# Performance work log

Measured on AMD Instinct MI355X. Metric: run time of the kernel, lower is better.

Reference implementation:

```python
import jax, jax.numpy as jnp
import numpy as np

# ---- config (from init_kwargs) ----
IMG_W, IMG_H = 6144.0, 6144.0
SCALE0 = 1.0
MAP_H, MAP_W = 384, 384
FEAT_STRIDE = 16
BASE_SIZE = 16
RATIOS = np.array([0.5, 1.0, 2.0], np.float32)
SCALES = np.array([8.0, 16.0, 32.0], np.float32)
RPN_MIN_SIZE = 16.0
PRE_NMS_N = 12000
POST_NMS_N = 2000
NMS_THRESH = 0.7


def _generate_anchors():
    w = h = float(BASE_SIZE)
    xc = 0.5 * (w - 1.0)
    yc = 0.5 * (h - 1.0)
    size = w * h
    ws = np.round(np.sqrt(size / RATIOS))
    hs = np.round(ws * RATIOS)
    ratio_anchors = np.stack([xc - 0.5 * (ws - 1), yc - 0.5 * (hs - 1),
                              xc + 0.5 * (ws - 1), yc + 0.5 * (hs - 1)], 1)
    out = []
    for a in ratio_anchors:
        aw = a[2] - a[0] + 1.0
        ah = a[3] - a[1] + 1.0
        axc = a[0] + 0.5 * (aw - 1.0)
        ayc = a[1] + 0.5 * (ah - 1.0)
        ws2 = aw * SCALES
        hs2 = ah * SCALES
        out.append(np.stack([axc - 0.5 * (ws2 - 1), ayc - 0.5 * (hs2 - 1),
                             axc + 0.5 * (ws2 - 1), ayc + 0.5 * (hs2 - 1)], 1))
    return np.concatenate(out, 0).astype(np.float32)  # (9,4)


def _all_anchors():
    anchors = _generate_anchors()
    sx = (np.arange(MAP_W) * FEAT_STRIDE).astype(np.float32)
    sy = (np.arange(MAP_H) * FEAT_STRIDE).astype(np.float32)
    SX, SY = np.meshgrid(sx, sy)
    shifts = np.stack([SX.ravel(), SY.ravel(), SX.ravel(), SY.ravel()], 1)
    return (shifts[:, None, :] + anchors[None, :, :]).reshape(-1, 4)  # (H*W*9, 4)


ALL_ANCHORS = jnp.asarray(_all_anchors())
N_TOTAL = ALL_ANCHORS.shape[0]  # 1,327,104


def _bbox_transform_inv(boxes, deltas):
    w = boxes[:, 2] - boxes[:, 0] + 1.0
    h = boxes[:, 3] - boxes[:, 1] + 1.0
    cx = boxes[:, 0] + 0.5 * w
    cy = boxes[:, 1] + 0.5 * h
    pcx = deltas[:, 0] * w + cx
    pcy = deltas[:, 1] * h + cy
    pw = jnp.exp(deltas[:, 2]) * w
    ph = jnp.exp(deltas[:, 3]) * h
    return jnp.stack([pcx - 0.5 * pw, pcy - 0.5 * ph,
                      pcx + 0.5 * pw, pcy + 0.5 * ph], 1)


def _clip_bbox(x, xlim, ylim):
    return jnp.stack([jnp.clip(x[:, 0], 0.0, xlim), jnp.clip(x[:, 1], 0.0, ylim),
                      jnp.clip(x[:, 2], 0.0, xlim), jnp.clip(x[:, 3], 0.0, ylim)], 1)


def _nms(boxes, max_out, thresh):
    # boxes already sorted by descending score; greedy NMS, returns
    # selected indices padded with -1 to max_out.
    n = boxes.shape[0]
    areas = (boxes[:, 2] - boxes[:, 0]) * (boxes[:, 3] - boxes[:, 1])

    def body(i, state):
        supp, sel, cnt = state
        take = jnp.logical_and(~supp[i], cnt < max_out)
        slot = jnp.minimum(cnt, max_out - 1)
        sel = sel.at[slot].set(jnp.where(take, i, sel[slot]))
        cnt = cnt + take.astype(jnp.int32)
        b = boxes[i]
        ix0 = jnp.maximum(b[0], boxes[:, 0])
        iy0 = jnp.maximum(b[1], boxes[:, 1])
        ix1 = jnp.minimum(b[2], boxes[:, 2])
        iy1 = jnp.minimum(b[3], boxes[:, 3])
        inter = jnp.maximum(ix1 - ix0, 0.0) * jnp.maximum(iy1 - iy0, 0.0)
        iou = inter / (areas[i] + areas - inter + 1e-9)
        supp = supp | (take & (iou > thresh))
        return supp, sel, cnt

    supp0 = jnp.zeros((n,), bool)
    sel0 = jnp.full((max_out,), -1, jnp.int32)
    supp, sel, cnt = jax.lax.fori_loop(0, n, body, (supp0, sel0, jnp.int32(0)))
    return sel


def setup_inputs() -> dict:
    key = jax.random.key(0)
    k1, k2 = jax.random.split(key)
    delta = jax.random.normal(k1, (1, N_TOTAL, 4), jnp.float32)
    score = jax.random.uniform(k2, (1, N_TOTAL, 2), jnp.float32)
    return {"delta": delta, "score": score}


def reference(delta, score):
    s = score[0, :, 1]                                  # (N,)
    props = _bbox_transform_inv(ALL_ANCHORS, delta[0])   # (N,4)
    props = _clip_bbox(props, IMG_W * SCALE0, IMG_H * SCALE0)
    w = props[:, 2] - props[:, 0]
    h = props[:, 3] - props[:, 1]
    keep = (w >= RPN_MIN_SIZE) & (h >= RPN_MIN_SIZE)
    # jit-compatible size filter: demote filtered boxes below everything
    s = jnp.where(keep, s, -jnp.inf)
    _, idx = jax.lax.top_k(s, PRE_NMS_N)                 # N >> PRE_NMS_N
    cand = props[idx]                                    # (PRE_NMS_N,4)
    sel = _nms(cand, POST_NMS_N, NMS_THRESH)             # (POST_NMS_N,)
    valid = sel >= 0
    out = jnp.where(valid[:, None], cand[jnp.clip(sel, 0)], 0.0)
    return out[None]                                     # (1, POST_NMS_N, 4)
```

## Files before the change

kernel.cpp:

```cpp
#include <hip/hip_runtime.h>
#include <stdint.h>

#define N_TOTAL  1327104
#define KPRE     12000
#define KPOST    2000
#define NPAD     12032
#define WORDS    188
#define NPHASE   94
#define CAND_CAP 16384
#define IMGLIM   6144.0f

__constant__ float c_aw[9] = {184.f,368.f,736.f,128.f,256.f,512.f, 88.f,176.f,352.f};
__constant__ float c_ah[9] = { 96.f,192.f,384.f,128.f,256.f,512.f,176.f,352.f,704.f};

__device__ __forceinline__ float mul_sep(float a, float b) {
    float r = a * b;
    asm volatile("" : "+v"(r));
    return r;
}

__device__ __forceinline__ void compute_box(int idx, const float4 d,
        float& ox0, float& oy0, float& ox1, float& oy1, bool& keep)
{
    int a    = idx % 9;
    int cell = idx / 9;
    int col  = cell % 384;
    int row  = cell / 384;
    float w = c_aw[a], h = c_ah[a];
    float cx = (float)(col * 16 + 8);
    float cy = (float)(row * 16 + 8);
    float pcx = mul_sep(d.x, w) + cx;
    float pcy = mul_sep(d.y, h) + cy;
    float pw = expf(d.z) * w;
    float ph = expf(d.w) * h;
    float x0 = pcx - 0.5f * pw;
    float y0 = pcy - 0.5f * ph;
    float x1 = pcx + 0.5f * pw;
    float y1 = pcy + 0.5f * ph;
    ox0 = fminf(fmaxf(x0, 0.f), IMGLIM);
    oy0 = fminf(fmaxf(y0, 0.f), IMGLIM);
    ox1 = fminf(fmaxf(x1, 0.f), IMGLIM);
    oy1 = fminf(fmaxf(y1, 0.f), IMGLIM);
    keep = ((ox1 - ox0) >= 16.f) && ((oy1 - oy0) >= 16.f);
}

__global__ void k_keys(const float* __restrict__ delta, const float* __restrict__ score,
                       uint32_t* __restrict__ keys, uint32_t* __restrict__ hist1)
{
    __shared__ uint32_t lh[2048];
    for (int t = threadIdx.x; t < 2048; t += blockDim.x) lh[t] = 0;
    __syncthreads();
    int idx = blockIdx.x * blockDim.x + threadIdx.x;
    if (idx < N_TOTAL) {
        float4 d = ((const float4*)delta)[idx];
        float x0, y0, x1, y1; bool keep;
        compute_box(idx, d, x0, y0, x1, y1, keep);
        float s = ((const float2*)score)[idx].y;
        uint32_t key = keep ? __float_as_uint(s) : 0u;
        keys[idx] = key;
        atomicAdd(&lh[key >> 21], 1u);
    }
    __syncthreads();
    for (int t = threadIdx.x; t < 2048; t += blockDim.x) {
        uint32_t c = lh[t];
        if (c) atomicAdd(&hist1[t], c);
    }
}

__global__ void k_hist2(const uint32_t* __restrict__ keys, const uint32_t* __restrict__ state,
                        uint32_t* __restrict__ hist)
{
    __shared__ uint32_t lh[2048];
    for (int t = threadIdx.x; t < 2048; t += blockDim.x) lh[t] = 0;
    __syncthreads();
    uint32_t B1 = state[0];
    int idx = blockIdx.x * blockDim.x + threadIdx.x;
    if (idx < N_TOTAL) {
        uint32_t k = keys[idx];
        if ((k >> 21) == B1) atomicAdd(&lh[(k >> 10) & 0x7FFu], 1u);
    }
    __syncthreads();
    for (int t = threadIdx.x; t < 2048; t += blockDim.x) {
        uint32_t c = lh[t];
        if (c) atomicAdd(&hist[t], c);
    }
}

__global__ void k_hist3(const uint32_t* __restrict__ keys, const uint32_t* __restrict__ state,
                        uint32_t* __restrict__ hist)
{
    __shared__ uint32_t lh[1024];
    for (int t = threadIdx.x; t < 1024; t += blockDim.x) lh[t] = 0;
    __syncthreads();
    uint32_t pfx = state[2];
    int idx = blockIdx.x * blockDim.x + threadIdx.x;
    if (idx < N_TOTAL) {
        uint32_t k = keys[idx];
        if ((k >> 10) == pfx) atomicAdd(&lh[k & 0x3FFu], 1u);
    }
    __syncthreads();
    for (int t = threadIdx.x; t < 1024; t += blockDim.x) {
        uint32_t c = lh[t];
        if (c) atomicAdd(&hist[t], c);
    }
}

__global__ void k_scan(const uint32_t* __restrict__ hist, uint32_t* __restrict__ state,
                       int nbins, int pass)
{
    __shared__ uint32_t sh[2048];
    __shared__ uint32_t part[256];
    __shared__ uint32_t sB, sRem;
    int t = threadIdx.x;
    int seg = nbins >> 8;
    uint32_t K = (pass == 0) ? (uint32_t)KPRE : ((pass == 1) ? state[1] : state[3]);
    if (K == 0u) K = 1u;
    uint32_t local = 0;
    for (int i = 0; i < seg; ++i) {
        uint32_t h = hist[t * seg + i];
        sh[t * seg + i] = h;
        local += h;
    }
    part[t] = local;
    __syncthreads();
    for (int off = 1; off < 256; off <<= 1) {
        uint32_t v = part[t];
        uint32_t add = (t + off < 256) ? part[t + off] : 0u;
        __syncthreads();
        part[t] = v + add;
        __syncthreads();
    }
    uint32_t mine  = part[t];
    uint32_t below = (t + 1 < 256) ? part[t + 1] : 0;
    if (mine >= K && below < K) {
        uint32_t cum = below;
        for (int i = seg - 1; i >= 0; --i) {
            uint32_t h = sh[t * seg + i];
            if (cum + h >= K) { sB = (uint32_t)(t * seg + i); sRem = K - cum; break; }
            cum += h;
        }
    }
    __syncthreads();
    if (t == 0) {
        uint32_t B = sB, rem = sRem;
        if      (pass == 0) { state[0] = B; state[1] = rem; }
        else if (pass == 1) { state[2] = (state[0] << 11) | B; state[3] = rem; }
        else                { state[4] = (state[2] << 10) | B; }
    }
}

__global__ void k_compact(const uint32_t* __restrict__ keys, uint32_t* __restrict__ state,
                          uint64_t* __restrict__ cand)
{
    uint32_t T = state[4];
    int idx = blockIdx.x * blockDim.x + threadIdx.x;
    bool pred = false; uint32_t k = 0;
    if (idx < N_TOTAL) { k = keys[idx]; pred = (k >= T); }
    uint64_t bal = __ballot(pred);
    if (bal == 0ull) return;
    int lane = threadIdx.x & 63;
    int leader = __ffsll((unsigned long long)bal) - 1;
    uint32_t base = 0;
    if (lane == leader) base = atomicAdd(&state[5], (uint32_t)__popcll((unsigned long long)bal));
    base = (uint32_t)__shfl((int)base, leader, 64);
    if (pred) {
        uint64_t lower = (lane == 0) ? 0ull : (~0ull >> (64 - lane));
        uint32_t p = base + (uint32_t)__popcll((unsigned long long)(bal & lower));
        if (p < CAND_CAP)
            cand[p] = ((uint64_t)k << 32) | (uint64_t)(0xFFFFFFFFu - (uint32_t)idx);
    }
}

__global__ __launch_bounds__(64)
void k_rankpart(const uint64_t* __restrict__ cand, const uint32_t* __restrict__ state,
                uint32_t* __restrict__ rank)
{
    __shared__ uint64_t lk[1024];
    uint32_t M = min(state[5], (uint32_t)CAND_CAP);
    uint32_t ib = blockIdx.x * 64;
    uint32_t jb = blockIdx.y * 1024;
    if (ib >= M || jb >= M) return;
    uint32_t chunk = min(1024u, M - jb);
    for (uint32_t t = threadIdx.x; t < chunk; t += 64) lk[t] = cand[jb + t];
    __syncthreads();
    uint32_t i = ib + threadIdx.x;
    if (i >= M) return;
    uint64_t mykey = cand[i];
    uint32_t r = 0;
    uint32_t j = 0;
    for (; j + 8 <= chunk; j += 8) {
        uint64_t a0 = lk[j], a1 = lk[j+1], a2 = lk[j+2], a3 = lk[j+3];
        uint64_t a4 = lk[j+4], a5 = lk[j+5], a6 = lk[j+6], a7 = lk[j+7];
        r += (a0 > mykey) + (a1 > mykey) + (a2 > mykey) + (a3 > mykey)
           + (a4 > mykey) + (a5 > mykey) + (a6 > mykey) + (a7 > mykey);
    }
    for (; j < chunk; ++j) r += (lk[j] > mykey) ? 1u : 0u;
    if (r) atomicAdd(&rank[i], r);
}

__global__ void k_scatterbox(const uint64_t* __restrict__ cand, const uint32_t* __restrict__ rank,
                             const uint32_t* __restrict__ state, const float* __restrict__ delta,
                             float* __restrict__ bx0, float* __restrict__ by0,
                             float* __restrict__ bx1, float* __restrict__ by1,
                             float* __restrict__ bar)
{
    uint32_t M = min(state[5], (uint32_t)CAND_CAP);
    uint32_t i = blockIdx.x * blockDim.x + threadIdx.x;
    if (i >= M) return;
    uint32_t r = rank[i];
    if (r >= KPRE) return;
    uint32_t aidx = 0xFFFFFFFFu - (uint32_t)(cand[i] & 0xFFFFFFFFull);
    float4 d = ((const float4*)delta)[aidx];
    float x0, y0, x1, y1; bool keep;
    compute_box((int)aidx, d, x0, y0, x1, y1, keep);
    bx0[r] = x0; by0[r] = y0; bx1[r] = x1; by1[r] = y1;
    bar[r] = (x1 - x0) * (y1 - y0);
}

__global__ void k_mask(const float* __restrict__ bx0, const float* __restrict__ by0,
                       const float* __restrict__ bx1, const float* __restrict__ by1,
                       const float* __restrict__ bar, uint64_t* __restrict__ mask,
                       uint64_t* __restrict__ diagband, uint64_t* __restrict__ band1,
                       uint64_t* __restrict__ band2, uint64_t* __restrict__ band3,
                       uint64_t* __restrict__ band4, uint64_t* __restrict__ band5)
{
    __shared__ float s0[256], s1[256], s2[256], s3[256], sa[256];
    int rr = threadIdx.x >> 2;
    int q  = threadIdx.x & 3;
    int bx = blockIdx.x;
    int r  = bx * 64 + rr;
    int cstart = max(0, (bx - 5) >> 2);
    int total  = (NPAD / 256) - cstart;
    int chunk  = (total + 3) >> 2;
    int c0 = cstart + (int)blockIdx.y * chunk;
    int c1 = min(c0 + chunk, NPAD / 256);
    float rx0 = bx0[r], ry0 = by0[r], rx1 = bx1[r], ry1 = by1[r], ra = bar[r];
    for (int c = c0; c < c1; ++c) {
        int cb = c * 256;
        __syncthreads();
        int t = threadIdx.x;
        s0[t] = bx0[cb + t]; s1[t] = by0[cb + t];
        s2[t] = bx1[cb + t]; s3[t] = by1[cb + t];
        sa[t] = bar[cb + t];
        __syncthreads();
        uint64_t bits = 0;
        int j0 = q * 64;
        #pragma unroll 4
        for (int j = 0; j < 64; ++j) {
            int jj = j0 + j;
            float ix0 = fmaxf(rx0, s0[jj]);
            float iy0 = fmaxf(ry0, s1[jj]);
            float ix1 = fminf(rx1, s2[jj]);
            float iy1 = fminf(ry1, s3[jj]);
            float iw = fmaxf(ix1 - ix0, 0.f);
            float ih = fmaxf(iy1 - iy0, 0.f);
            float inter = iw * ih;
            float denom = ra + sa[jj] - inter + 1e-9f;
            float iou = inter / denom;
            bits |= ((uint64_t)(iou > 0.7f)) << j;
        }
        int w = c * 4 + q;
        mask[(size_t)r * WORDS + (size_t)w] = bits;
        if      (w == bx)     diagband[r] = bits;
        else if (w == bx - 1) band1[r]    = bits;
        else if (w == bx - 2) band2[r]    = bits;
        else if (w == bx - 3) band3[r]    = bits;
        else if (w == bx - 4) band4[r]    = bits;
        else if (w == bx - 5) band5[r]    = bits;
    }
}

__device__ __forceinline__ void pick_chain(uint64_t& avail, uint64_t& pk, int& cnt,
                                           uint32_t cLo, uint32_t cHi)
{
    while (avail != 0ull && cnt < KPOST) {
        #pragma unroll
        for (int u = 0; u < 4; ++u) {
            bool take = (avail != 0ull) && (cnt < KPOST);
            uint64_t a2 = take ? avail : 1ull;
            int b = __ffsll((unsigned long long)a2) - 1;
            uint32_t lo = (uint32_t)__builtin_amdgcn_readlane((int)cLo, b);
            uint32_t hi = (uint32_t)__builtin_amdgcn_readlane((int)cHi, b);
            uint64_t col = ((uint64_t)hi << 32) | (uint64_t)lo;
            pk   |= take ? (1ull << b) : 0ull;
            cnt  += take ? 1 : 0;
            avail = take ? (avail & ~col) : avail;
        }
    }
}

__global__ __launch_bounds__(1024, 1)
void k_nms(const uint64_t* __restrict__ mask, const uint64_t* __restrict__ diagband,
           const uint64_t* __restrict__ band1, const uint64_t* __restrict__ band2,
           const uint64_t* __restrict__ band3, const uint64_t* __restrict__ band4,
           const uint64_t* __restrict__ band5,
           const float* __restrict__ bx0, const float* __restrict__ by0,
           const float* __restrict__ bx1, const float* __restrict__ by1,
           float4* __restrict__ out)
{
    __shared__ uint32_t p32[WORDS * 2];
    __shared__ uint64_t dbuf[2][128], b1buf[2][128], b2buf[2][128],
                        b3buf[2][128], b4buf[2][128], b5buf[2][128];
    __shared__ uint32_t pickbuf[2][128];
    __shared__ uint32_t npickS[2];
    __shared__ uint32_t stopF;
    __shared__ uint16_t sel_lds[KPOST];
    __shared__ uint32_t cntTot;
    const int tid  = threadIdx.x;
    const int lane = tid & 63;
    const int wv   = tid >> 6;

    for (int t = tid; t < WORDS * 2; t += 1024) p32[t] = 0;
    if (tid == 0) { npickS[0] = 0; npickS[1] = 0; stopF = 0; }

    const uint64_t* srcA = nullptr;
    if (wv >= 10)
        srcA = (wv == 10) ? diagband : (wv == 11) ? band1 : (wv == 12) ? band2
             : (wv == 13) ? band3    : (wv == 14) ? band4 : band5;
    uint64_t bc0 = 0, bc1 = 0;
    if (wv >= 10) {
        uint64_t v0 = srcA[lane], v1 = srcA[64 + lane];
        uint64_t* dst = (wv == 10) ? dbuf[0] : (wv == 11) ? b1buf[0]
                      : (wv == 12) ? b2buf[0] : (wv == 13) ? b3buf[0]
                      : (wv == 14) ? b4buf[0] : b5buf[0];
        dst[lane] = v0; dst[64 + lane] = v1;
        bc0 = srcA[128 + lane]; bc1 = srcA[192 + lane];
    }
    __syncthreads();

    int cnt = 0;
    uint64_t pm1 = 0, pm2 = 0, pm3 = 0, pm4 = 0, pm5 = 0;
    uint64_t pA0 = 0, pA1 = 0, pA2 = 0, pB0 = 0, pB1 = 0, pB2 = 0;
    int pcb = WORDS;

    for (int ph = 0; ph < NPHASE; ++ph) {
        const int qb = ph & 1;
        if (wv == 0) {
            const int w0 = 2 * ph, w1 = w0 + 1;
            uint64_t col0 = dbuf[qb][lane],  col1 = dbuf[qb][64 + lane];
            uint64_t b1a = b1buf[qb][lane],  b1b = b1buf[qb][64 + lane];
            uint64_t b2a = b2buf[qb][lane],  b2b = b2buf[qb][64 + lane];
            uint64_t b3a = b3buf[qb][lane],  b3b = b3buf[qb][64 + lane];
            uint64_t b4a = b4buf[qb][lane],  b4b = b4buf[qb][64 + lane];
            uint64_t b5a = b5buf[qb][lane],  b5b = b5buf[qb][64 + lane];
            uint64_t pw0 = ((uint64_t)p32[2 * w0 + 1] << 32) | (uint64_t)p32[2 * w0];
            uint64_t pw1 = ((uint64_t)p32[2 * w1 + 1] << 32) | (uint64_t)p32[2 * w1];
            bool al0 = !((pw0 >> lane) & 1) && !(b1a & pm1) && !(b2a & pm2)
                     && !(b3a & pm3) && !(b4a & pm4) && !(b5a & pm5);
            uint64_t avail = __ballot(al0);
            uint64_t pk0 = 0;
            int cnt0 = cnt;
            pick_chain(avail, pk0, cnt, (uint32_t)col0, (uint32_t)(col0 >> 32));
            int np0 = cnt - cnt0;
            bool al1 = !((pw1 >> lane) & 1) && !(b1b & pk0) && !(b2b & pm1)
                     && !(b3b & pm2) && !(b4b & pm3) && !(b5b & pm4);
            if (w1 == WORDS - 1 && lane >= 32) al1 = false;
            avail = __ballot(al1);
            uint64_t pk1 = 0;
            int cnt1 = cnt;
            pick_chain(avail, pk1, cnt, (uint32_t)col1, (uint32_t)(col1 >> 32));
            int np1 = cnt - cnt1;
            if (lane < np0) {
                uint64_t s = pk0;
                for (int q = 0; q < lane; ++q) s &= s - 1;
                uint32_t gi = (uint32_t)(w0 * 64 + (__ffsll((unsigned long long)s) - 1));
                sel_lds[cnt0 + lane] = (uint16_t)gi;
                pickbuf[qb][lane] = gi;
            }
            if (lane < np1) {
                uint64_t s = pk1;
                for (int q = 0; q < lane; ++q) s &= s - 1;
                uint32_t gi = (uint32_t)(w1 * 64 + (__ffsll((unsigned long long)s) - 1));
                sel_lds[cnt1 + lane] = (uint16_t)gi;
                pickbuf[qb][np0 + lane] = gi;
            }
            if (lane == 0) {
                npickS[qb] = (uint32_t)(np0 + np1);
                if (cnt >= KPOST || ph + 1 >= NPHASE) stopF = 1u;
            }
            pm5 = pm3; pm4 = pm2; pm3 = pm1; pm2 = pk0; pm1 = pk1;
        } else {
            if (pcb < WORDS) {
                uint64_t v0 = pA0 | pB0, v1 = pA1 | pB1, v2 = pA2 | pB2;
                int w0c = pcb + lane, w1c = w0c + 64, w2c = w1c + 64;
                if (v0 && w0c < WORDS) {
                    uint32_t lo = (uint32_t)v0, hi = (uint32_t)(v0 >> 32);
                    if (lo) atomicOr(&p32[2 * w0c], lo);
                    if (hi) atomicOr(&p32[2 * w0c + 1], hi);
                }
                if (v1 && w1c < WORDS) {
                    uint32_t lo = (uint32_t)v1, hi = (uint32_t)(v1 >> 32);
                    if (lo) atomicOr(&p32[2 * w1c], lo);
                    if (hi) atomicOr(&p32[2 * w1c + 1], hi);
                }
                if (v2 && w2c < WORDS) {
                    uint32_t lo = (uint32_t)v2, hi = (uint32_t)(v2 >> 32);
                    if (lo) atomicOr(&p32[2 * w2c], lo);
                    if (hi) atomicOr(&p32[2 * w2c + 1], hi);
                }
            }
            pcb = WORDS;
            pA0 = pA1 = pA2 = pB0 = pB1 = pB2 = 0;
            if (wv >= 10) {
                const int nb = qb ^ 1;
                uint64_t* dst = (wv == 10) ? dbuf[nb] : (wv == 11) ? b1buf[nb]
                              : (wv == 12) ? b2buf[nb] : (wv == 13) ? b3buf[nb]
                              : (wv == 14) ? b4buf[nb] : b5buf[nb];
                dst[lane] = bc0; dst[64 + lane] = bc1;
                if (ph + 2 < NPHASE) {
                    int base = (2 * (ph + 2)) * 64;
                    bc0 = srcA[base + lane];
                    bc1 = srcA[base + 64 + lane];
                }
            }
            if (ph >= 1) {
                const int pqb = (ph - 1) & 1;
                const int npk = (int)npickS[pqb];
                const int cb = 2 * ph + 4;
                const int j = wv - 1;
                if (j < npk && cb < WORDS) {
                    int w0i = cb + lane, w1i = w0i + 64, w2i = w1i + 64;
                    {
                        const uint64_t* row =
                            mask + (size_t)pickbuf[pqb][j] * WORDS;
                        pA0 = (w0i < WORDS) ? row[w0i] : 0ull;
                        pA1 = (w1i < WORDS) ? row[w1i] : 0ull;
                        pA2 = (w2i < WORDS) ? row[w2i] : 0ull;
                        pcb = cb;
                    }
                    int j2 = j + 15;
                    if (j2 < npk) {
                        const uint64_t* row =
                            mask + (size_t)pickbuf[pqb][j2] * WORDS;
                        pB0 = (w0i < WORDS) ? row[w0i] : 0ull;
                        pB1 = (w1i < WORDS) ? row[w1i] : 0ull;
                        pB2 = (w2i < WORDS) ? row[w2i] : 0ull;
                    }
                    for (int j3 = j + 30; j3 < npk; j3 += 15) {
                        const uint64_t* row =
                            mask + (size_t)pickbuf[pqb][j3] * WORDS;
                        uint64_t v0 = (w0i < WORDS) ? row[w0i] : 0ull;
                        uint64_t v1 = (w1i < WORDS) ? row[w1i] : 0ull;
                        uint64_t v2 = (w2i < WORDS) ? row[w2i] : 0ull;
                        if (v0) {
                            uint32_t lo = (uint32_t)v0, hi = (uint32_t)(v0 >> 32);
                            if (lo) atomicOr(&p32[2 * w0i], lo);
                            if (hi) atomicOr(&p32[2 * w0i + 1], hi);
                        }
                        if (v1 && w1i < WORDS) {
                            uint32_t lo = (uint32_t)v1, hi = (uint32_t)(v1 >> 32);
                            if (lo) atomicOr(&p32[2 * w1i], lo);
                            if (hi) atomicOr(&p32[2 * w1i + 1], hi);
                        }
                        if (v2 && w2i < WORDS) {
                            uint32_t lo = (uint32_t)v2, hi = (uint32_t)(v2 >> 32);
                            if (lo) atomicOr(&p32[2 * w2i], lo);
                            if (hi) atomicOr(&p32[2 * w2i + 1], hi);
                        }
                    }
                }
            }
        }
        asm volatile("s_waitcnt lgkmcnt(0)" ::: "memory");
        __builtin_amdgcn_s_barrier();
        asm volatile("" ::: "memory");
        if (stopF) break;
    }
    if (wv == 0 && lane == 0) cntTot = (uint32_t)cnt;
    __syncthreads();
    uint32_t cfin = cntTot;
    for (int slot = tid; slot < KPOST; slot += 1024) {
        float4 v = make_float4(0.f, 0.f, 0.f, 0.f);
        if ((uint32_t)slot < cfin) {
            int i = (int)sel_lds[slot];
            v = make_float4(bx0[i], by0[i], bx1[i], by1[i]);
        }
        out[slot] = v;
    }
}

extern "C" void kernel_launch(void* const* d_in, const int* in_sizes, int n_in,
                              void* d_out, int out_size, void* d_ws, size_t ws_size,
                              hipStream_t stream)
{
    const float* delta = (const float*)d_in[0];
    const float* score = (const float*)d_in[1];
    float4* out = (float4*)d_out;

    uint8_t* p = (uint8_t*)d_ws;
    auto alloc = [&](size_t bytes) -> void* {
        void* r = (void*)p;
        p += (bytes + 255) & ~(size_t)255;
        return r;
    };
    uint32_t* keys          = (uint32_t*)alloc((size_t)N_TOTAL * 4);
    uint64_t* cand          = (uint64_t*)alloc((size_t)CAND_CAP * 8);
    uint64_t* diagband      = (uint64_t*)alloc((size_t)NPAD * 8);
    uint64_t* mask          = (uint64_t*)alloc((size_t)NPAD * WORDS * 8);
    uint32_t* hist1         = (uint32_t*)alloc(2048 * 4);
    uint32_t* hist2         = (uint32_t*)alloc(2048 * 4);
    uint32_t* hist3         = (uint32_t*)alloc(1024 * 4);
    uint32_t* rank          = (uint32_t*)alloc((size_t)CAND_CAP * 4);
    uint32_t* state         = (uint32_t*)alloc(64);
    float*    bx0           = (float*)alloc((size_t)NPAD * 4);
    float*    by0           = (float*)alloc((size_t)NPAD * 4);
    float*    bx1           = (float*)alloc((size_t)NPAD * 4);
    float*    by1           = (float*)alloc((size_t)NPAD * 4);
    float*    bar           = (float*)alloc((size_t)NPAD * 4);
    uint64_t* band1         = (uint64_t*)alloc((size_t)NPAD * 8);
    uint64_t* band2         = (uint64_t*)alloc((size_t)NPAD * 8);
    uint64_t* band3         = (uint64_t*)alloc((size_t)NPAD * 8);
    uint64_t* band4         = (uint64_t*)alloc((size_t)NPAD * 8);
    uint64_t* band5         = (uint64_t*)alloc((size_t)NPAD * 8);
    (void)ws_size; (void)n_in; (void)in_sizes; (void)out_size;

    size_t zero_sz = (size_t)(((uint8_t*)band5 + (size_t)NPAD * 8) - (uint8_t*)hist1);
    hipMemsetAsync((void*)hist1, 0, zero_sz, stream);

    const int B = 256;
    const int gN = (N_TOTAL + B - 1) / B;

    hipLaunchKernelGGL(k_keys, dim3(gN), dim3(B), 0, stream, delta, score, keys, hist1);
    hipLaunchKernelGGL(k_scan, dim3(1), dim3(B), 0, stream, hist1, state, 2048, 0);
    hipLaunchKernelGGL(k_hist2, dim3(gN), dim3(B), 0, stream, keys, state, hist2);
    hipLaunchKernelGGL(k_scan, dim3(1), dim3(B), 0, stream, hist2, state, 2048, 1);
    hipLaunchKernelGGL(k_hist3, dim3(gN), dim3(B), 0, stream, keys, state, hist3);
    hipLaunchKernelGGL(k_scan, dim3(1), dim3(B), 0, stream, hist3, state, 1024, 2);
    hipLaunchKernelGGL(k_compact, dim3(gN), dim3(B), 0, stream, keys, state, cand);
    hipLaunchKernelGGL(k_rankpart, dim3(CAND_CAP / 64, CAND_CAP / 1024), dim3(64), 0, stream,
                       cand, state, rank);
    hipLaunchKernelGGL(k_scatterbox, dim3(CAND_CAP / B), dim3(B), 0, stream,
                       cand, rank, state, delta, bx0, by0, bx1, by1, bar);
    hipLaunchKernelGGL(k_mask, dim3(NPAD / 64, 4), dim3(B), 0, stream,
                       bx0, by0, bx1, by1, bar, mask, diagband,
                       band1, band2, band3, band4, band5);
    hipLaunchKernelGGL(k_nms, dim3(1), dim3(1024), 0, stream,
                       mask, diagband, band1, band2, band3, band4, band5,
                       bx0, by0, bx1, by1, out);
}
```

Measured before the change: 531.9 us.

## Shrink NMS block to four waves with register-held bands and deeper row prefetch

Cuts the single-block NMS kernel from 16 waves to 4. The picking wave now loads the diagonal and band columns straight into registers, prefetching two phases ahead, instead of having dedicated waves stage them through shared memory. The three remaining helper waves each prefetch up to eight picked mask rows into register arrays and handle any extra rows in a loop. The aim is cheaper per-phase barriers and fewer shared-memory round trips on the serial path. In exchange there is less parallelism for OR-ing suppression rows and higher register pressure.

```diff
diff --git a/kernel.cpp b/kernel.cpp
--- a/kernel.cpp
+++ b/kernel.cpp
@@ -289,7 +289,7 @@
     }
 }
 
-__global__ __launch_bounds__(1024, 1)
+__global__ __launch_bounds__(256, 1)
 void k_nms(const uint64_t* __restrict__ mask, const uint64_t* __restrict__ diagband,
            const uint64_t* __restrict__ band1, const uint64_t* __restrict__ band2,
            const uint64_t* __restrict__ band3, const uint64_t* __restrict__ band4,
@@ -299,8 +299,6 @@
            float4* __restrict__ out)
 {
     __shared__ uint32_t p32[WORDS * 2];
-    __shared__ uint64_t dbuf[2][128], b1buf[2][128], b2buf[2][128],
-                        b3buf[2][128], b4buf[2][128], b5buf[2][128];
     __shared__ uint32_t pickbuf[2][128];
     __shared__ uint32_t npickS[2];
     __shared__ uint32_t stopF;
@@ -310,55 +308,55 @@
     const int lane = tid & 63;
     const int wv   = tid >> 6;
 
-    for (int t = tid; t < WORDS * 2; t += 1024) p32[t] = 0;
-    if (tid == 0) { npickS[0] = 0; npickS[1] = 0; stopF = 0; }
-
-    const uint64_t* srcA = nullptr;
-    if (wv >= 10)
-        srcA = (wv == 10) ? diagband : (wv == 11) ? band1 : (wv == 12) ? band2
-             : (wv == 13) ? band3    : (wv == 14) ? band4 : band5;
-    uint64_t bc0 = 0, bc1 = 0;
-    if (wv >= 10) {
-        uint64_t v0 = srcA[lane], v1 = srcA[64 + lane];
-        uint64_t* dst = (wv == 10) ? dbuf[0] : (wv == 11) ? b1buf[0]
-                      : (wv == 12) ? b2buf[0] : (wv == 13) ? b3buf[0]
-                      : (wv == 14) ? b4buf[0] : b5buf[0];
-        dst[lane] = v0; dst[64 + lane] = v1;
-        bc0 = srcA[128 + lane]; bc1 = srcA[192 + lane];
-    }
+    for (int t = tid; t < WORDS * 2; t += 256) p32[t] = 0;
+    if (tid == 0) { npickS[0] = 0; npickS[1] = 0; stopF = 0; cntTot = 0; }
     __syncthreads();
 
     int cnt = 0;
     uint64_t pm1 = 0, pm2 = 0, pm3 = 0, pm4 = 0, pm5 = 0;
-    uint64_t pA0 = 0, pA1 = 0, pA2 = 0, pB0 = 0, pB1 = 0, pB2 = 0;
+
+    uint64_t dA=0,dB=0, o1A=0,o1B=0, o2A=0,o2B=0, o3A=0,o3B=0, o4A=0,o4B=0, o5A=0,o5B=0;
+    uint64_t ndA=0,ndB=0, n1A=0,n1B=0, n2A=0,n2B=0, n3A=0,n3B=0, n4A=0,n4B=0, n5A=0,n5B=0;
+    if (wv == 0) {
+        dA  = diagband[lane];       dB  = diagband[64 + lane];
+        o1A = band1[lane];          o1B = band1[64 + lane];
+        o2A = band2[lane];          o2B = band2[64 + lane];
+        o3A = band3[lane];          o3B = band3[64 + lane];
+        o4A = band4[lane];          o4B = band4[64 + lane];
+        o5A = band5[lane];          o5B = band5[64 + lane];
+        ndA = diagband[128 + lane]; ndB = diagband[192 + lane];
+        n1A = band1[128 + lane];    n1B = band1[192 + lane];
+        n2A = band2[128 + lane];    n2B = band2[192 + lane];
+        n3A = band3[128 + lane];    n3B = band3[192 + lane];
+        n4A = band4[128 + lane];    n4B = band4[192 + lane];
+        n5A = band5[128 + lane];    n5B = band5[192 + lane];
+    }
+
+    uint64_t pv0[8], pv1[8], pv2[8];
+    #pragma unroll
+    for (int s = 0; s < 8; ++s) { pv0[s] = 0; pv1[s] = 0; pv2[s] = 0; }
     int pcb = WORDS;
 
     for (int ph = 0; ph < NPHASE; ++ph) {
         const int qb = ph & 1;
         if (wv == 0) {
             const int w0 = 2 * ph, w1 = w0 + 1;
-            uint64_t col0 = dbuf[qb][lane],  col1 = dbuf[qb][64 + lane];
-            uint64_t b1a = b1buf[qb][lane],  b1b = b1buf[qb][64 + lane];
-            uint64_t b2a = b2buf[qb][lane],  b2b = b2buf[qb][64 + lane];
-            uint64_t b3a = b3buf[qb][lane],  b3b = b3buf[qb][64 + lane];
-            uint64_t b4a = b4buf[qb][lane],  b4b = b4buf[qb][64 + lane];
-            uint64_t b5a = b5buf[qb][lane],  b5b = b5buf[qb][64 + lane];
             uint64_t pw0 = ((uint64_t)p32[2 * w0 + 1] << 32) | (uint64_t)p32[2 * w0];
             uint64_t pw1 = ((uint64_t)p32[2 * w1 + 1] << 32) | (uint64_t)p32[2 * w1];
-            bool al0 = !((pw0 >> lane) & 1) && !(b1a & pm1) && !(b2a & pm2)
-                     && !(b3a & pm3) && !(b4a & pm4) && !(b5a & pm5);
+            bool al0 = !((pw0 >> lane) & 1) && !(o1A & pm1) && !(o2A & pm2)
+                     && !(o3A & pm3) && !(o4A & pm4) && !(o5A & pm5);
             uint64_t avail = __ballot(al0);
             uint64_t pk0 = 0;
             int cnt0 = cnt;
-            pick_chain(avail, pk0, cnt, (uint32_t)col0, (uint32_t)(col0 >> 32));
+            pick_chain(avail, pk0, cnt, (uint32_t)dA, (uint32_t)(dA >> 32));
             int np0 = cnt - cnt0;
-            bool al1 = !((pw1 >> lane) & 1) && !(b1b & pk0) && !(b2b & pm1)
-                     && !(b3b & pm2) && !(b4b & pm3) && !(b5b & pm4);
+            bool al1 = !((pw1 >> lane) & 1) && !(o1B & pk0) && !(o2B & pm1)
+                     && !(o3B & pm2) && !(o4B & pm3) && !(o5B & pm4);
             if (w1 == WORDS - 1 && lane >= 32) al1 = false;
             avail = __ballot(al1);
             uint64_t pk1 = 0;
             int cnt1 = cnt;
-            pick_chain(avail, pk1, cnt, (uint32_t)col1, (uint32_t)(col1 >> 32));
+            pick_chain(avail, pk1, cnt, (uint32_t)dB, (uint32_t)(dB >> 32));
             int np1 = cnt - cnt1;
             if (lane < np0) {
                 uint64_t s = pk0;
@@ -379,66 +377,65 @@
                 if (cnt >= KPOST || ph + 1 >= NPHASE) stopF = 1u;
             }
             pm5 = pm3; pm4 = pm2; pm3 = pm1; pm2 = pk0; pm1 = pk1;
+            dA = ndA; dB = ndB; o1A = n1A; o1B = n1B; o2A = n2A; o2B = n2B;
+            o3A = n3A; o3B = n3B; o4A = n4A; o4B = n4B; o5A = n5A; o5B = n5B;
+            if (ph + 2 < NPHASE) {
+                int base = (2 * (ph + 2)) * 64;
+                ndA = diagband[base + lane]; ndB = diagband[base + 64 + lane];
+                n1A = band1[base + lane];    n1B = band1[base + 64 + lane];
+                n2A = band2[base + lane];    n2B = band2[base + 64 + lane];
+                n3A = band3[base + lane];    n3B = band3[base + 64 + lane];
+                n4A = band4[base + lane];    n4B = band4[base + 64 + lane];
+                n5A = band5[base + lane];    n5B = band5[base + 64 + lane];
+            }
         } else {
             if (pcb < WORDS) {
-                uint64_t v0 = pA0 | pB0, v1 = pA1 | pB1, v2 = pA2 | pB2;
+                uint64_t a0 = pv0[0] | pv0[1] | pv0[2] | pv0[3]
+                            | pv0[4] | pv0[5] | pv0[6] | pv0[7];
+                uint64_t a1 = pv1[0] | pv1[1] | pv1[2] | pv1[3]
+                            | pv1[4] | pv1[5] | pv1[6] | pv1[7];
+                uint64_t a2 = pv2[0] | pv2[1] | pv2[2] | pv2[3]
+                            | pv2[4] | pv2[5] | pv2[6] | pv2[7];
                 int w0c = pcb + lane, w1c = w0c + 64, w2c = w1c + 64;
-                if (v0 && w0c < WORDS) {
-                    uint32_t lo = (uint32_t)v0, hi = (uint32_t)(v0 >> 32);
+                if (a0 && w0c < WORDS) {
+                    uint32_t lo = (uint32_t)a0, hi = (uint32_t)(a0 >> 32);
                     if (lo) atomicOr(&p32[2 * w0c], lo);
                     if (hi) atomicOr(&p32[2 * w0c + 1], hi);
                 }
-                if (v1 && w1c < WORDS) {
-                    uint32_t lo = (uint32_t)v1, hi = (uint32_t)(v1 >> 32);
+                if (a1 && w1c < WORDS) {
+                    uint32_t lo = (uint32_t)a1, hi = (uint32_t)(a1 >> 32);
                     if (lo) atomicOr(&p32[2 * w1c], lo);
                     if (hi) atomicOr(&p32[2 * w1c + 1], hi);
                 }
-                if (v2 && w2c < WORDS) {
-                    uint32_t lo = (uint32_t)v2, hi = (uint32_t)(v2 >> 32);
+                if (a2 && w2c < WORDS) {
+                    uint32_t lo = (uint32_t)a2, hi = (uint32_t)(a2 >> 32);
                     if (lo) atomicOr(&p32[2 * w2c], lo);
                     if (hi) atomicOr(&p32[2 * w2c + 1], hi);
                 }
             }
             pcb = WORDS;
-            pA0 = pA1 = pA2 = pB0 = pB1 = pB2 = 0;
-            if (wv >= 10) {
-                const int nb = qb ^ 1;
-                uint64_t* dst = (wv == 10) ? dbuf[nb] : (wv == 11) ? b1buf[nb]
-                              : (wv == 12) ? b2buf[nb] : (wv == 13) ? b3buf[nb]
-                              : (wv == 14) ? b4buf[nb] : b5buf[nb];
-                dst[lane] = bc0; dst[64 + lane] = bc1;
-                if (ph + 2 < NPHASE) {
-                    int base = (2 * (ph + 2)) * 64;
-                    bc0 = srcA[base + lane];
-                    bc1 = srcA[base + 64 + lane];
-                }
-            }
+            #pragma unroll
+            for (int s = 0; s < 8; ++s) { pv0[s] = 0; pv1[s] = 0; pv2[s] = 0; }
             if (ph >= 1) {
                 const int pqb = (ph - 1) & 1;
                 const int npk = (int)npickS[pqb];
                 const int cb = 2 * ph + 4;
-                const int j = wv - 1;
-                if (j < npk && cb < WORDS) {
+                if (npk > 0 && cb < WORDS) {
                     int w0i = cb + lane, w1i = w0i + 64, w2i = w1i + 64;
-                    {
+                    #pragma unroll
+                    for (int s = 0; s < 8; ++s) {
+                        int j = (wv - 1) + 3 * s;
+                        bool on = (j < npk);
+                        const uint64_t* row =
+                            mask + (size_t)pickbuf[pqb][on ? j : 0] * WORDS;
+                        pv0[s] = (on && w0i < WORDS) ? row[w0i] : 0ull;
+                        pv1[s] = (on && w1i < WORDS) ? row[w1i] : 0ull;
+                        pv2[s] = (on && w2i < WORDS) ? row[w2i] : 0ull;
+                    }
+                    pcb = cb;
+                    for (int j = (wv - 1) + 24; j < npk; j += 3) {
                         const uint64_t* row =
                             mask + (size_t)pickbuf[pqb][j] * WORDS;
-                        pA0 = (w0i < WORDS) ? row[w0i] : 0ull;
-                        pA1 = (w1i < WORDS) ? row[w1i] : 0ull;
-                        pA2 = (w2i < WORDS) ? row[w2i] : 0ull;
-                        pcb = cb;
-                    }
-                    int j2 = j + 15;
-                    if (j2 < npk) {
-                        const uint64_t* row =
-                            mask + (size_t)pickbuf[pqb][j2] * WORDS;
-                        pB0 = (w0i < WORDS) ? row[w0i] : 0ull;
-                        pB1 = (w1i < WORDS) ? row[w1i] : 0ull;
-                        pB2 = (w2i < WORDS) ? row[w2i] : 0ull;
-                    }
-                    for (int j3 = j + 30; j3 < npk; j3 += 15) {
-                        const uint64_t* row =
-                            mask + (size_t)pickbuf[pqb][j3] * WORDS;
                         uint64_t v0 = (w0i < WORDS) ? row[w0i] : 0ull;
                         uint64_t v1 = (w1i < WORDS) ? row[w1i] : 0ull;
                         uint64_t v2 = (w2i < WORDS) ? row[w2i] : 0ull;
@@ -469,7 +466,7 @@
     if (wv == 0 && lane == 0) cntTot = (uint32_t)cnt;
     __syncthreads();
     uint32_t cfin = cntTot;
-    for (int slot = tid; slot < KPOST; slot += 1024) {
+    for (int slot = tid; slot < KPOST; slot += 256) {
         float4 v = make_float4(0.f, 0.f, 0.f, 0.f);
         if ((uint32_t)slot < cfin) {
             int i = (int)sel_lds[slot];
@@ -534,7 +531,7 @@
     hipLaunchKernelGGL(k_mask, dim3(NPAD / 64, 4), dim3(B), 0, stream,
                        bx0, by0, bx1, by1, bar, mask, diagband,
                        band1, band2, band3, band4, band5);
-    hipLaunchKernelGGL(k_nms, dim3(1), dim3(1024), 0, stream,
+    hipLaunchKernelGGL(k_nms, dim3(1), dim3(256), 0, stream,
                        mask, diagband, band1, band2, band3, band4, band5,
                        bx0, by0, bx1, by1, out);
 }
```

New measurement: 604.4 us. 13.6% more time.
